# Kernel optimization log

Hardware: AMD Instinct MI355X
Metric: run time of the kernel (lower is better)

The kernel has to match this reference:

```python
import jax, jax.numpy as jnp
import numpy as np

D_K = 64  # hardcoded in source module

def setup_inputs() -> dict:
    key = jax.random.key(0)
    kq, kk, kv, km = jax.random.split(key, 4)
    B, H, S, D = 2, 16, 2048, D_K
    Q = jax.random.normal(kq, (B, H, S, D), dtype=jnp.float32)
    K = jax.random.normal(kk, (B, H, S, D), dtype=jnp.float32)
    V = jax.random.normal(kv, (B, H, S, D), dtype=jnp.float32)
    # boolean mask: True positions are masked out (filled with -1e9)
    attn_mask = jax.random.randint(km, (B, H, S, S), 0, 2) == 1
    return {"Q": Q, "K": K, "V": V, "attn_mask": attn_mask}

def reference(Q, K, V, attn_mask):
    scale = 1.0 / np.sqrt(D_K).astype(np.float32)
    # scores: [B, H, S, S]
    scores = jnp.einsum('bhqd,bhkd->bhqk', Q, K) * scale
    scores = jnp.where(attn_mask, jnp.float32(-1e9), scores)
    attn = jax.nn.softmax(scores, axis=-1)
    context = jnp.einsum('bhqk,bhkd->bhqd', attn, V)
    return context
```

## Files before the change

### kernel.cpp

```cpp
#include <hip/hip_runtime.h>

#define SEQ   2048
#define DK    64
#define QBLK  64
#define KVBLK 64
#define NTILE (SEQ / KVBLK)
#define PITCH 72

typedef __attribute__((ext_vector_type(8))) __bf16 bf16x8;
typedef __attribute__((ext_vector_type(4))) __bf16 bf16x4;
typedef __attribute__((ext_vector_type(4))) float  f32x4;
typedef __attribute__((ext_vector_type(4))) int    i32x4;

__device__ __forceinline__ float grp16_max(float v) {
  v = fmaxf(v, __shfl_xor(v, 1));
  v = fmaxf(v, __shfl_xor(v, 2));
  v = fmaxf(v, __shfl_xor(v, 4));
  v = fmaxf(v, __shfl_xor(v, 8));
  return v;
}
__device__ __forceinline__ float grp16_sum(float v) {
  v += __shfl_xor(v, 1);
  v += __shfl_xor(v, 2);
  v += __shfl_xor(v, 4);
  v += __shfl_xor(v, 8);
  return v;
}

__device__ __forceinline__ void block_sync_lds() {
  asm volatile("s_waitcnt lgkmcnt(0)" ::: "memory");
  __builtin_amdgcn_sched_barrier(0);
  __builtin_amdgcn_s_barrier();
  __builtin_amdgcn_sched_barrier(0);
}

struct KState {
  const float* Kp; const float* Vp; const int* Mp;
  int sk, sd, sj, g, li, w, q0;
};

__global__ __launch_bounds__(256, 2)
void sdpa_fwd(const float* __restrict__ Q, const float* __restrict__ K,
              const float* __restrict__ V, const int* __restrict__ M,
              float* __restrict__ O)
{
  __shared__ __bf16 Klds[KVBLK][PITCH];
  __shared__ __bf16 Vt[DK][PITCH];
  __shared__ __bf16 Plds[4][16][PITCH];

  const int tid  = threadIdx.x;
  const int w    = tid >> 6;
  const int lane = tid & 63;
  const int g    = lane >> 4;
  const int li   = lane & 15;

  const int bid = blockIdx.x;
  const int blk = (bid & 7) * 128 + (bid >> 3);
  const int qb  = blk & (SEQ / QBLK - 1);
  const int bh  = blk >> 5;

  const float* Qp = Q + (size_t)bh * SEQ * DK;
  const float* Kp = K + (size_t)bh * SEQ * DK;
  const float* Vp = V + (size_t)bh * SEQ * DK;
  const int*   Mp = M + (size_t)bh * SEQ * SEQ;
  float*       Op = O + (size_t)bh * SEQ * DK;

  const int q0 = qb * QBLK + w * 16;

  const int sk = tid >> 2;
  const int sd = (tid & 3) * 16;
  const int sj = ((sk & 3) << 4) | (sk >> 2);

  bf16x8 qfrag[2];
  {
    const float qs = 0.125f * 1.44269504088896340736f;
    const float* qr = Qp + (size_t)(q0 + li) * DK + g * 8;
    #pragma unroll
    for (int h2 = 0; h2 < 2; ++h2) {
      f32x4 a = *(const f32x4*)(qr + h2 * 32);
      f32x4 b = *(const f32x4*)(qr + h2 * 32 + 4);
      bf16x8 f;
      #pragma unroll
      for (int e = 0; e < 4; ++e) { f[e] = (__bf16)(a[e] * qs); f[4 + e] = (__bf16)(b[e] * qs); }
      qfrag[h2] = f;
    }
  }

  f32x4 acc[4];
  #pragma unroll
  for (int c = 0; c < 4; ++c) acc[c] = (f32x4){0.f, 0.f, 0.f, 0.f};
  float m_r[4], l_r[4];
  #pragma unroll
  for (int r = 0; r < 4; ++r) { m_r[r] = -__builtin_inff(); l_r[r] = 0.f; }

  f32x4 kA[4], vA[4];
  i32x4 mA[4], mB[4];

  {
    const float* ks = Kp + (size_t)sk * DK + sd;
    const float* vs = Vp + (size_t)sk * DK + sd;
    #pragma unroll
    for (int i = 0; i < 4; ++i) { kA[i] = *(const f32x4*)(ks + 4 * i); vA[i] = *(const f32x4*)(vs + 4 * i); }
    #pragma unroll
    for (int r = 0; r < 4; ++r) {
      const size_t mrow = (size_t)(q0 + 4 * g + r) * SEQ + li * 4;
      mA[r] = *(const i32x4*)(Mp + mrow);
      mB[r] = *(const i32x4*)(Mp + mrow + KVBLK);
    }
  }

  auto body = [&](int kt, i32x4 (&mc)[4], i32x4 (&mn)[4]) {
    block_sync_lds();

    {
      bf16x8 klo, khi;
      #pragma unroll
      for (int e = 0; e < 4; ++e) {
        klo[e] = (__bf16)kA[0][e]; klo[4 + e] = (__bf16)kA[1][e];
        khi[e] = (__bf16)kA[2][e]; khi[4 + e] = (__bf16)kA[3][e];
      }
      *(bf16x8*)&Klds[sj][sd]     = klo;
      *(bf16x8*)&Klds[sj][sd + 8] = khi;
      #pragma unroll
      for (int qd = 0; qd < 4; ++qd)
        #pragma unroll
        for (int e = 0; e < 4; ++e)
          Vt[sd + qd * 4 + e][sk] = (__bf16)vA[qd][e];
    }

    i32x4 msk[4];
    #pragma unroll
    for (int r = 0; r < 4; ++r) msk[r] = mc[r];

    {
      const int tm = (kt + 2 < NTILE) ? kt + 2 : 0;
      #pragma unroll
      for (int r = 0; r < 4; ++r)
        mc[r] = *(const i32x4*)(Mp + (size_t)(q0 + 4 * g + r) * SEQ + tm * KVBLK + li * 4);
      const int tn = (kt + 1 < NTILE) ? kt + 1 : 0;
      const float* ks = Kp + (size_t)(tn * KVBLK + sk) * DK + sd;
      const float* vs = Vp + (size_t)(tn * KVBLK + sk) * DK + sd;
      #pragma unroll
      for (int i = 0; i < 4; ++i) { kA[i] = *(const f32x4*)(ks + 4 * i); vA[i] = *(const f32x4*)(vs + 4 * i); }
    }

    block_sync_lds();

    f32x4 st[4];
    #pragma unroll
    for (int nt = 0; nt < 4; ++nt) {
      bf16x8 b0 = *(const bf16x8*)&Klds[nt * 16 + li][g * 8];
      bf16x8 b1 = *(const bf16x8*)&Klds[nt * 16 + li][32 + g * 8];
      f32x4 s = (f32x4){0.f, 0.f, 0.f, 0.f};
      s = __builtin_amdgcn_mfma_f32_16x16x32_bf16(qfrag[0], b0, s, 0, 0, 0);
      s = __builtin_amdgcn_mfma_f32_16x16x32_bf16(qfrag[1], b1, s, 0, 0, 0);
      st[nt] = s;
    }

    #pragma unroll
    for (int r = 0; r < 4; ++r) {
      float s0 = msk[r].x ? -1e9f : st[0][r];
      float s1 = msk[r].y ? -1e9f : st[1][r];
      float s2 = msk[r].z ? -1e9f : st[2][r];
      float s3 = msk[r].w ? -1e9f : st[3][r];
      float mx    = grp16_max(fmaxf(fmaxf(s0, s1), fmaxf(s2, s3)));
      float mnew  = fmaxf(m_r[r], mx);
      float alpha = __builtin_amdgcn_exp2f(m_r[r] - mnew);
      float p0 = __builtin_amdgcn_exp2f(s0 - mnew);
      float p1 = __builtin_amdgcn_exp2f(s1 - mnew);
      float p2 = __builtin_amdgcn_exp2f(s2 - mnew);
      float p3 = __builtin_amdgcn_exp2f(s3 - mnew);
      l_r[r] = l_r[r] * alpha + grp16_sum((p0 + p1) + (p2 + p3));
      m_r[r] = mnew;
      acc[0][r] *= alpha;
      acc[1][r] *= alpha;
      acc[2][r] *= alpha;
      acc[3][r] *= alpha;
      bf16x4 pk;
      pk[0] = (__bf16)p0; pk[1] = (__bf16)p1; pk[2] = (__bf16)p2; pk[3] = (__bf16)p3;
      *(bf16x4*)&Plds[w][4 * g + r][li * 4] = pk;
    }

    asm volatile("s_waitcnt lgkmcnt(0)" ::: "memory");
    __builtin_amdgcn_sched_barrier(0);

    bf16x8 pa0 = *(const bf16x8*)&Plds[w][li][g * 8];
    bf16x8 pa1 = *(const bf16x8*)&Plds[w][li][32 + g * 8];
    #pragma unroll
    for (int dt = 0; dt < 4; ++dt) {
      bf16x8 v0 = *(const bf16x8*)&Vt[dt * 16 + li][g * 8];
      bf16x8 v1 = *(const bf16x8*)&Vt[dt * 16 + li][32 + g * 8];
      acc[dt] = __builtin_amdgcn_mfma_f32_16x16x32_bf16(pa0, v0, acc[dt], 0, 0, 0);
      acc[dt] = __builtin_amdgcn_mfma_f32_16x16x32_bf16(pa1, v1, acc[dt], 0, 0, 0);
    }
  };

  for (int kt = 0; kt < NTILE; kt += 2) {
    body(kt, mA, mB);
    body(kt + 1, mB, mA);
  }

  #pragma unroll
  for (int r = 0; r < 4; ++r) {
    float inv = 1.0f / l_r[r];
    float* orow = Op + (size_t)(q0 + 4 * g + r) * DK + li;
    #pragma unroll
    for (int dt = 0; dt < 4; ++dt)
      orow[dt * 16] = acc[dt][r] * inv;
  }
}

extern "C" void kernel_launch(void* const* d_in, const int* in_sizes, int n_in,
                              void* d_out, int out_size, void* d_ws, size_t ws_size,
                              hipStream_t stream) {
  const float* Q = (const float*)d_in[0];
  const float* K = (const float*)d_in[1];
  const float* V = (const float*)d_in[2];
  const int*   M = (const int*)d_in[3];
  float*       O = (float*)d_out;

  const int nblocks = 2 * 16 * (SEQ / QBLK);
  sdpa_fwd<<<nblocks, 256, 0, stream>>>(Q, K, V, M, O);
}
```

Measured before the change: 768.2 us.

## Use DPP row reductions, packed V transpose stores, setprio and higher occupancy

```diff
diff --git a/kernel.cpp b/kernel.cpp
--- a/kernel.cpp
+++ b/kernel.cpp
@@ -9,21 +9,28 @@
 
 typedef __attribute__((ext_vector_type(8))) __bf16 bf16x8;
 typedef __attribute__((ext_vector_type(4))) __bf16 bf16x4;
+typedef __attribute__((ext_vector_type(2))) __bf16 bf16x2;
 typedef __attribute__((ext_vector_type(4))) float  f32x4;
 typedef __attribute__((ext_vector_type(4))) int    i32x4;
 
+template<int CTRL>
+__device__ __forceinline__ float dpp_ror(float v) {
+  int i = __builtin_bit_cast(int, v);
+  int r = __builtin_amdgcn_update_dpp(i, i, CTRL, 0xf, 0xf, false);
+  return __builtin_bit_cast(float, r);
+}
 __device__ __forceinline__ float grp16_max(float v) {
-  v = fmaxf(v, __shfl_xor(v, 1));
-  v = fmaxf(v, __shfl_xor(v, 2));
-  v = fmaxf(v, __shfl_xor(v, 4));
-  v = fmaxf(v, __shfl_xor(v, 8));
+  v = fmaxf(v, dpp_ror<0x128>(v));
+  v = fmaxf(v, dpp_ror<0x124>(v));
+  v = fmaxf(v, dpp_ror<0x122>(v));
+  v = fmaxf(v, dpp_ror<0x121>(v));
   return v;
 }
 __device__ __forceinline__ float grp16_sum(float v) {
-  v += __shfl_xor(v, 1);
-  v += __shfl_xor(v, 2);
-  v += __shfl_xor(v, 4);
-  v += __shfl_xor(v, 8);
+  v += dpp_ror<0x128>(v);
+  v += dpp_ror<0x124>(v);
+  v += dpp_ror<0x122>(v);
+  v += dpp_ror<0x121>(v);
   return v;
 }
 
@@ -34,12 +41,7 @@
   __builtin_amdgcn_sched_barrier(0);
 }
 
-struct KState {
-  const float* Kp; const float* Vp; const int* Mp;
-  int sk, sd, sj, g, li, w, q0;
-};
-
-__global__ __launch_bounds__(256, 2)
+__global__ __launch_bounds__(256, 3)
 void sdpa_fwd(const float* __restrict__ Q, const float* __restrict__ K,
               const float* __restrict__ V, const int* __restrict__ M,
               float* __restrict__ O)
@@ -70,6 +72,8 @@
   const int sk = tid >> 2;
   const int sd = (tid & 3) * 16;
   const int sj = ((sk & 3) << 4) | (sk >> 2);
+  const int vk = (tid & 31) * 2;
+  const int vd = (tid >> 5) * 8;
 
   bf16x8 qfrag[2];
   {
@@ -97,10 +101,13 @@
   i32x4 mA[4], mB[4];
 
   {
-    const float* ks = Kp + (size_t)sk * DK + sd;
-    const float* vs = Vp + (size_t)sk * DK + sd;
-    #pragma unroll
-    for (int i = 0; i < 4; ++i) { kA[i] = *(const f32x4*)(ks + 4 * i); vA[i] = *(const f32x4*)(vs + 4 * i); }
+    const float* ks  = Kp + (size_t)sk * DK + sd;
+    const float* vs0 = Vp + (size_t)vk * DK + vd;
+    const float* vs1 = Vp + (size_t)(vk + 1) * DK + vd;
+    #pragma unroll
+    for (int i = 0; i < 4; ++i) kA[i] = *(const f32x4*)(ks + 4 * i);
+    vA[0] = *(const f32x4*)vs0; vA[1] = *(const f32x4*)(vs0 + 4);
+    vA[2] = *(const f32x4*)vs1; vA[3] = *(const f32x4*)(vs1 + 4);
     #pragma unroll
     for (int r = 0; r < 4; ++r) {
       const size_t mrow = (size_t)(q0 + 4 * g + r) * SEQ + li * 4;
@@ -109,7 +116,7 @@
     }
   }
 
-  auto body = [&](int kt, i32x4 (&mc)[4], i32x4 (&mn)[4]) {
+  auto body = [&](int kt, i32x4 (&mc)[4]) {
     block_sync_lds();
 
     {
@@ -122,31 +129,36 @@
       *(bf16x8*)&Klds[sj][sd]     = klo;
       *(bf16x8*)&Klds[sj][sd + 8] = khi;
       #pragma unroll
-      for (int qd = 0; qd < 4; ++qd)
-        #pragma unroll
-        for (int e = 0; e < 4; ++e)
-          Vt[sd + qd * 4 + e][sk] = (__bf16)vA[qd][e];
+      for (int j = 0; j < 4; ++j) {
+        bf16x2 p0; p0[0] = (__bf16)vA[0][j]; p0[1] = (__bf16)vA[2][j];
+        bf16x2 p1; p1[0] = (__bf16)vA[1][j]; p1[1] = (__bf16)vA[3][j];
+        *(bf16x2*)&Vt[vd + j][vk]     = p0;
+        *(bf16x2*)&Vt[vd + 4 + j][vk] = p1;
+      }
     }
 
     i32x4 msk[4];
     #pragma unroll
     for (int r = 0; r < 4; ++r) msk[r] = mc[r];
-
     {
       const int tm = (kt + 2 < NTILE) ? kt + 2 : 0;
       #pragma unroll
       for (int r = 0; r < 4; ++r)
         mc[r] = *(const i32x4*)(Mp + (size_t)(q0 + 4 * g + r) * SEQ + tm * KVBLK + li * 4);
       const int tn = (kt + 1 < NTILE) ? kt + 1 : 0;
-      const float* ks = Kp + (size_t)(tn * KVBLK + sk) * DK + sd;
-      const float* vs = Vp + (size_t)(tn * KVBLK + sk) * DK + sd;
-      #pragma unroll
-      for (int i = 0; i < 4; ++i) { kA[i] = *(const f32x4*)(ks + 4 * i); vA[i] = *(const f32x4*)(vs + 4 * i); }
+      const float* ks  = Kp + (size_t)(tn * KVBLK + sk) * DK + sd;
+      const float* vs0 = Vp + (size_t)(tn * KVBLK + vk) * DK + vd;
+      const float* vs1 = Vp + (size_t)(tn * KVBLK + vk + 1) * DK + vd;
+      #pragma unroll
+      for (int i = 0; i < 4; ++i) kA[i] = *(const f32x4*)(ks + 4 * i);
+      vA[0] = *(const f32x4*)vs0; vA[1] = *(const f32x4*)(vs0 + 4);
+      vA[2] = *(const f32x4*)vs1; vA[3] = *(const f32x4*)(vs1 + 4);
     }
 
     block_sync_lds();
 
     f32x4 st[4];
+    __builtin_amdgcn_s_setprio(1);
     #pragma unroll
     for (int nt = 0; nt < 4; ++nt) {
       bf16x8 b0 = *(const bf16x8*)&Klds[nt * 16 + li][g * 8];
@@ -156,6 +168,7 @@
       s = __builtin_amdgcn_mfma_f32_16x16x32_bf16(qfrag[1], b1, s, 0, 0, 0);
       st[nt] = s;
     }
+    __builtin_amdgcn_s_setprio(0);
 
     #pragma unroll
     for (int r = 0; r < 4; ++r) {
@@ -186,6 +199,7 @@
 
     bf16x8 pa0 = *(const bf16x8*)&Plds[w][li][g * 8];
     bf16x8 pa1 = *(const bf16x8*)&Plds[w][li][32 + g * 8];
+    __builtin_amdgcn_s_setprio(1);
     #pragma unroll
     for (int dt = 0; dt < 4; ++dt) {
       bf16x8 v0 = *(const bf16x8*)&Vt[dt * 16 + li][g * 8];
@@ -193,11 +207,12 @@
       acc[dt] = __builtin_amdgcn_mfma_f32_16x16x32_bf16(pa0, v0, acc[dt], 0, 0, 0);
       acc[dt] = __builtin_amdgcn_mfma_f32_16x16x32_bf16(pa1, v1, acc[dt], 0, 0, 0);
     }
+    __builtin_amdgcn_s_setprio(0);
   };
 
   for (int kt = 0; kt < NTILE; kt += 2) {
-    body(kt, mA, mB);
-    body(kt + 1, mB, mA);
+    body(kt, mA);
+    body(kt + 1, mB);
   }
 
   #pragma unroll
```

After: 856.2 us. 11.5% more time.
